# Performance work log

Hardware: AMD Instinct MI355X
Metric: run time of the kernel (lower is better)

The kernel has to match this reference:

```python
import jax, jax.numpy as jnp
import numpy as np


def _exp_levels(dx, depth):
    """Tensor-algebra exponential of a single increment dx [B, C]:
    level j is dx^{(x) j} / j!, flattened to [B, C^j]."""
    B = dx.shape[0]
    levels = [dx]
    for j in range(2, depth + 1):
        levels.append((jnp.einsum('bi,bj->bij', levels[-1], dx) / j).reshape(B, -1))
    return levels


def _chen_step(levels, dx, depth):
    """Chen's identity: sig(path * segment) = sig(path) (x) exp(dx).
    levels: tuple of [B, C^k] for k=1..depth. dx: [B, C]."""
    B = dx.shape[0]
    exps = _exp_levels(dx, depth)
    new = []
    for k in range(1, depth + 1):
        acc = levels[k - 1] + exps[k - 1]  # A_k * 1  +  1 * E_k
        for j in range(1, k):
            # A_{k-j} (x) E_j, flattened: [B, C^{k-j}] x [B, C^j] -> [B, C^k]
            acc = acc + jnp.einsum('bi,bj->bij', levels[k - j - 1], exps[j - 1]).reshape(B, -1)
        new.append(acc)
    return tuple(new)


def setup_inputs() -> dict:
    key = jax.random.key(0)
    path = jax.random.normal(key, (64, 512, 10), dtype=jnp.float32)
    return {"path": path, "depth": 4}


def reference(path, depth):
    # signature(path, depth, stream=False, basepoint=False, inverse=False,
    #           initial=None, scalar_term=False)
    dx = path[:, 1:] - path[:, :-1]  # [B, L-1, C] increments
    B = path.shape[0]
    # Initialise with the signature of the first segment: exp(dx_0).
    init = tuple(_exp_levels(dx[:, 0], depth))
    # Fold remaining segments via Chen's relation (a sequential scan; the
    # original's batch-trick is just a reassociation of this same product).
    dx_rest = jnp.swapaxes(dx[:, 1:], 0, 1)  # [L-2, B, C]

    def step(carry, d):
        return _chen_step(carry, d, depth), None

    carry, _ = jax.lax.scan(step, init, dx_rest)
    # Concatenate levels: output [B, C + C^2 + ... + C^depth]
    return jnp.concatenate(carry, axis=-1)
```

## Files before the change

### kernel.cpp

```cpp
#include <hip/hip_runtime.h>


#define CH      10
#define NSTEPS  511
#define ROW     12
#define SIGSZ   11110

__global__ __launch_bounds__(256, 1)
void sig_kernel(const float* __restrict__ path, float* __restrict__ out) {
    __shared__ __align__(16) float dxL[NSTEPS * ROW];

    const int tid  = threadIdx.x;
    const int b    = blockIdx.x >> 2;
    const int part = blockIdx.x & 3;

    const float* p = path + b * (512 * CH);
    for (int e = tid; e < NSTEPS * CH; e += 256) {
        int s = e / CH;
        int c = e - s * CH;
        dxL[s * ROW + c] = p[e + CH] - p[e];
    }
    __syncthreads();

    const int id = part * 256 + tid;
    if (id < 1000) {
        const int ci = id / 100;
        const int cj = (id / 10) % 10;
        const int ck = id % 10;

        float a1 = 0.f, a2 = 0.f, a3 = 0.f;
        float a4[10];
        #pragma unroll
        for (int l = 0; l < 10; ++l) a4[l] = 0.f;

        #pragma unroll 4
        for (int s = 0; s < NSTEPS; ++s) {
            const float* row = dxL + s * ROW;
            const float4 d0 = *(const float4*)(row);
            const float4 d1 = *(const float4*)(row + 4);
            const float2 d2 = *(const float2*)(row + 8);
            const float dxi = row[ci];
            const float dxj = row[cj];
            const float dxk = row[ck];

            const float p1 = a1 * (1.f / 6.f)  + dxi * (1.f / 24.f);
            const float q1 = a1 * 0.5f         + dxi * (1.f / 6.f);
            const float r1 = a1                + dxi * 0.5f;
            const float p2 = a2 * 0.5f + p1 * dxj;
            const float q2 = a2        + q1 * dxj;
            a2 += r1 * dxj;
            const float p3 = a3 + p2 * dxk;
            a3 += q2 * dxk;
            a1 += dxi;

            a4[0] += p3 * d0.x; a4[1] += p3 * d0.y;
            a4[2] += p3 * d0.z; a4[3] += p3 * d0.w;
            a4[4] += p3 * d1.x; a4[5] += p3 * d1.y;
            a4[6] += p3 * d1.z; a4[7] += p3 * d1.w;
            a4[8] += p3 * d2.x; a4[9] += p3 * d2.y;
        }

        float* ob = out + b * SIGSZ;
        float* o4 = ob + 1110 + id * 10;
        #pragma unroll
        for (int l = 0; l < 10; ++l) o4[l] = a4[l];
        ob[110 + id] = a3;
        if (ck == 0)            ob[10 + ci * 10 + cj] = a2;
        if (ck == 0 && cj == 0) ob[ci] = a1;
    }
}

extern "C" void kernel_launch(void* const* d_in, const int* in_sizes, int n_in,
                              void* d_out, int out_size, void* d_ws, size_t ws_size,
                              hipStream_t stream) {
    const float* path = (const float*)d_in[0];
    float* out = (float*)d_out;
    sig_kernel<<<dim3(256), dim3(256), 0, stream>>>(path, out);
}
```

Measured before the change: 102.0 us.

## Split path into segments computed in parallel and combine via Chen's identity

Divides the 511 increments into four segments of 128 steps, each computed by its own block on a 2D grid, and writes the partial signatures to workspace. A second kernel then merges the segment signatures per output element using Chen's tensor product. This multiplies grid parallelism from 256 blocks to 1024 and shortens the sequential dependency chain. The cost is an extra launch, workspace traffic, and the combine arithmetic. It relies on d_ws being large enough.

```diff
diff --git a/kernel.cpp b/kernel.cpp
--- a/kernel.cpp
+++ b/kernel.cpp
@@ -5,20 +5,25 @@
 #define NSTEPS  511
 #define ROW     12
 #define SIGSZ   11110
+#define NSEG    4
+#define SEGLEN  128
+#define WSSEG   11112
 
-__global__ __launch_bounds__(256, 1)
-void sig_kernel(const float* __restrict__ path, float* __restrict__ out) {
-    __shared__ __align__(16) float dxL[NSTEPS * ROW];
+__global__ __launch_bounds__(256)
+void sig_partial(const float* __restrict__ path, float* __restrict__ ws) {
+    __shared__ __align__(16) float dxL[SEGLEN * ROW];
 
     const int tid  = threadIdx.x;
     const int b    = blockIdx.x >> 2;
     const int part = blockIdx.x & 3;
+    const int seg  = blockIdx.y;
+    const int s0   = seg * SEGLEN;
 
-    const float* p = path + b * (512 * CH);
-    for (int e = tid; e < NSTEPS * CH; e += 256) {
+    const float* p = path + b * (512 * CH) + s0 * CH;
+    for (int e = tid; e < SEGLEN * CH; e += 256) {
         int s = e / CH;
         int c = e - s * CH;
-        dxL[s * ROW + c] = p[e + CH] - p[e];
+        dxL[s * ROW + c] = (s0 + s < NSTEPS) ? (p[e + CH] - p[e]) : 0.f;
     }
     __syncthreads();
 
@@ -34,7 +39,7 @@
         for (int l = 0; l < 10; ++l) a4[l] = 0.f;
 
         #pragma unroll 4
-        for (int s = 0; s < NSTEPS; ++s) {
+        for (int s = 0; s < SEGLEN; ++s) {
             const float* row = dxL + s * ROW;
             const float4 d0 = *(const float4*)(row);
             const float4 d1 = *(const float4*)(row + 4);
@@ -60,7 +65,7 @@
             a4[8] += p3 * d2.x; a4[9] += p3 * d2.y;
         }
 
-        float* ob = out + b * SIGSZ;
+        float* ob = ws + (b * NSEG + seg) * WSSEG;
         float* o4 = ob + 1110 + id * 10;
         #pragma unroll
         for (int l = 0; l < 10; ++l) o4[l] = a4[l];
@@ -70,10 +75,70 @@
     }
 }
 
+__global__ __launch_bounds__(256)
+void sig_combine(const float* __restrict__ ws, float* __restrict__ out) {
+    const int tid  = threadIdx.x;
+    const int b    = blockIdx.x >> 2;
+    const int part = blockIdx.x & 3;
+    const int id   = part * 256 + tid;
+    if (id >= 1000) return;
+
+    const int ci = id / 100;
+    const int cj = (id / 10) % 10;
+    const int ck = id % 10;
+
+    const float* w0 = ws + b * NSEG * WSSEG;
+
+    float a1 = w0[ci];
+    float a2 = w0[10 + ci * 10 + cj];
+    float a3 = w0[110 + id];
+    float a4[10];
+    #pragma unroll
+    for (int l = 0; l < 10; ++l) a4[l] = w0[1110 + id * 10 + l];
+
+    #pragma unroll
+    for (int s = 1; s < NSEG; ++s) {
+        const float* wb = w0 + s * WSSEG;
+        const float b1i   = wb[ci];
+        const float b1j   = wb[cj];
+        const float b1k   = wb[ck];
+        const float b2_ij = wb[10 + ci * 10 + cj];
+        const float b2_jk = wb[10 + cj * 10 + ck];
+        const float b3ijk = wb[110 + id];
+
+        float b1v[10], b2k[10], b3jk[10], b4v[10];
+        #pragma unroll
+        for (int l = 0; l < 10; ++l) {
+            b1v[l]  = wb[l];
+            b2k[l]  = wb[10 + ck * 10 + l];
+            b3jk[l] = wb[110 + (cj * 10 + ck) * 10 + l];
+            b4v[l]  = wb[1110 + id * 10 + l];
+        }
+
+        #pragma unroll
+        for (int l = 0; l < 10; ++l)
+            a4[l] += a3 * b1v[l] + a2 * b2k[l] + a1 * b3jk[l] + b4v[l];
+        a3 += a2 * b1k + a1 * b2_jk + b3ijk;
+        a2 += a1 * b1j + b2_ij;
+        a1 += b1i;
+    }
+
+    float* ob = out + b * SIGSZ;
+    float* o4 = ob + 1110 + id * 10;
+    #pragma unroll
+    for (int l = 0; l < 10; ++l) o4[l] = a4[l];
+    ob[110 + id] = a3;
+    if (ck == 0)            ob[10 + ci * 10 + cj] = a2;
+    if (ck == 0 && cj == 0) ob[ci] = a1;
+}
+
 extern "C" void kernel_launch(void* const* d_in, const int* in_sizes, int n_in,
                               void* d_out, int out_size, void* d_ws, size_t ws_size,
                               hipStream_t stream) {
     const float* path = (const float*)d_in[0];
     float* out = (float*)d_out;
-    sig_kernel<<<dim3(256), dim3(256), 0, stream>>>(path, out);
+    float* ws  = (float*)d_ws;
+
+    sig_partial<<<dim3(256, NSEG), dim3(256), 0, stream>>>(path, ws);
+    sig_combine<<<dim3(256), dim3(256), 0, stream>>>(ws, out);
 }
```

After: 89.82 us. -12.0%, faster.
